# Kernel optimization log

Hardware: AMD Instinct MI355X
Metric: run time of the kernel (lower is better)

Reference implementation:

```python
import jax, jax.numpy as jnp
import numpy as np

N_NODES = 100000
N_EDGES = 1600000
HID = 32


def gcn_conv(x, W, b, src, dst, num_nodes):
    # PyG GCNConv: h = X W; out = D^{-1/2}(A+I)D^{-1/2} h + b
    # (self loops already appended to src/dst by caller)
    h = x @ W
    deg = jax.ops.segment_sum(jnp.ones_like(dst, dtype=h.dtype), dst,
                              num_segments=num_nodes)
    dinv = jnp.where(deg > 0, jax.lax.rsqrt(deg), 0.0)
    norm = dinv[src] * dinv[dst]                      # [E+N]
    msg = h[src] * norm[:, None]                      # gather + scale
    out = jax.ops.segment_sum(msg, dst, num_segments=num_nodes)  # scatter-add
    return out + b


def setup_inputs() -> dict:
    key = jax.random.key(0)
    ks = jax.random.split(key, 12)
    x = jax.random.normal(ks[0], (N_NODES, 2), dtype=jnp.float32)
    edge_index = jax.random.randint(ks[1], (2, N_EDGES), 0, N_NODES,
                                    dtype=jnp.int32)
    s = 0.2  # small init scale
    return {
        "x": x,
        "edge_index": edge_index,
        "fc1_W": jax.random.normal(ks[2], (2, HID), jnp.float32) * s,
        "fc1_b": jnp.zeros((HID,), jnp.float32),
        "c1_W": jax.random.normal(ks[3], (HID, HID), jnp.float32) * s,
        "c1_b": jnp.zeros((HID,), jnp.float32),
        "c2_W": jax.random.normal(ks[4], (HID, HID), jnp.float32) * s,
        "c2_b": jnp.zeros((HID,), jnp.float32),
        "c3_W": jax.random.normal(ks[5], (HID, HID), jnp.float32) * s,
        "c3_b": jnp.zeros((HID,), jnp.float32),
        "fc2_W": jax.random.normal(ks[6], (HID, HID), jnp.float32) * s,
        "fc2_b": jnp.zeros((HID,), jnp.float32),
        "fc3_W": jax.random.normal(ks[7], (HID, 1), jnp.float32) * s,
        "fc3_b": jnp.zeros((1,), jnp.float32),
    }


def reference(x, edge_index, fc1_W, fc1_b, c1_W, c1_b, c2_W, c2_b,
              c3_W, c3_b, fc2_W, fc2_b, fc3_W, fc3_b):
    num_nodes = x.shape[0]
    loop = jnp.arange(num_nodes, dtype=edge_index.dtype)
    src = jnp.concatenate([edge_index[0], loop])  # add self loops
    dst = jnp.concatenate([edge_index[1], loop])
    h = jax.nn.relu(x @ fc1_W + fc1_b)
    h = jax.nn.relu(gcn_conv(h, c1_W, c1_b, src, dst, num_nodes))
    h = jax.nn.relu(gcn_conv(h, c2_W, c2_b, src, dst, num_nodes))
    h = jax.nn.relu(gcn_conv(h, c3_W, c3_b, src, dst, num_nodes))
    h = jax.nn.relu(h @ fc2_W + fc2_b)
    return h @ fc3_W + fc3_b
```

## Files before the change

kernel.cpp:

```cpp
#include <hip/hip_runtime.h>
#include <hip/hip_fp16.h>

#define NN 100000
#define NE 1600000
#define HID 32
#define NBK 391
#define CAP 4608
#define CHUNK 8192

__device__ __forceinline__ float4 load_h4(const __half* p) {
    uint2 u = *(const uint2*)p;
    __half2 h0 = *(__half2*)&u.x;
    __half2 h1 = *(__half2*)&u.y;
    float2 a = __half22float2(h0);
    float2 b = __half22float2(h1);
    return make_float4(a.x, a.y, b.x, b.y);
}

__global__ __launch_bounds__(256) void partA_kernel(
        const int* __restrict__ src, const int* __restrict__ dst,
        int* __restrict__ bktcur, int* __restrict__ bedges) {
    __shared__ int cache[CHUNK];
    __shared__ int hist[NBK];
    __shared__ int lofs[NBK];
    int t = threadIdx.x;
    int base = blockIdx.x * CHUNK;
    for (int i = t; i < NBK; i += 256) hist[i] = 0;
    __syncthreads();
    for (int i = t; i < CHUNK; i += 256) {
        int e = base + i;
        if (e < NE) {
            int d = dst[e];
            cache[i] = d;
            atomicAdd(&hist[d >> 8], 1);
        }
    }
    __syncthreads();
    for (int i = t; i < NBK; i += 256)
        lofs[i] = hist[i] ? atomicAdd(&bktcur[i], hist[i]) : 0;
    __syncthreads();
    for (int i = t; i < CHUNK; i += 256) {
        int e = base + i;
        if (e < NE) {
            int d = cache[i];
            int s = src[e];
            int b = d >> 8;
            int rel = atomicAdd(&lofs[b], 1);
            if (rel < CAP) bedges[b * CAP + rel] = (s << 8) | (d & 255);
        }
    }
}

__global__ __launch_bounds__(256) void bucket_csr_kernel(
        const int* __restrict__ bedges, const int* __restrict__ bktcur,
        const float* __restrict__ x, float* __restrict__ dinv,
        int* __restrict__ srcidx, int* __restrict__ rbeg, int* __restrict__ rend,
        float4* __restrict__ xpack) {
    __shared__ int ldeg[256];
    __shared__ int lcur[256];
    __shared__ int wsum[256];
    int b = blockIdx.x, t = threadIdx.x;
    int ebeg = b * CAP;
    int cnt = min(bktcur[b], CAP);
    int n0 = b << 8;
    ldeg[t] = 0;
    __syncthreads();
    for (int e = t; e < cnt; e += 256)
        atomicAdd(&ldeg[bedges[ebeg + e] & 255], 1);
    __syncthreads();
    int a = ldeg[t];
    wsum[t] = a;
    __syncthreads();
    for (int off = 1; off < 256; off <<= 1) {
        int xv = (t >= off) ? wsum[t - off] : 0;
        __syncthreads();
        wsum[t] += xv;
        __syncthreads();
    }
    int excl = wsum[t] - a;
    lcur[t] = excl;
    int n = n0 + t;
    if (n < NN) {
        float dv = rsqrtf((float)(a + 1));
        rbeg[n] = ebeg + excl;
        rend[n] = ebeg + excl + a;
        dinv[n] = dv;
        float2 xv2 = *(const float2*)&x[2 * n];
        xpack[n] = make_float4(xv2.x, xv2.y, dv, 0.f);
    }
    __syncthreads();
    for (int e = t; e < cnt; e += 256) {
        int w = bedges[ebeg + e];
        int pos = atomicAdd(&lcur[w & 255], 1);
        srcidx[ebeg + pos] = (unsigned)w >> 8;
    }
}

__global__ __launch_bounds__(256) void conv1_kernel(
        const float4* __restrict__ xpack, const int* __restrict__ rbeg,
        const int* __restrict__ rend, const int* __restrict__ srcidx,
        const float* __restrict__ dinv, const float* __restrict__ W1,
        const float* __restrict__ b1, const float* __restrict__ W,
        const float* __restrict__ bias, __half* __restrict__ hs_out) {
    __shared__ float wl[HID * HID];
    __shared__ float agg[8][HID];
    int tid = threadIdx.x;
    int base8 = blockIdx.x * 8;
#pragma unroll
    for (int i = 0; i < 4; ++i) wl[tid + 256 * i] = W[tid + 256 * i];
    int wave = tid >> 6, lane = tid & 63;
    int g = lane >> 3;
    int l = lane & 7;
    float4 w0q = *(const float4*)&W1[l << 2];
    float4 w1q = *(const float4*)&W1[HID + (l << 2)];
    float4 bq  = *(const float4*)&b1[l << 2];
#pragma unroll
    for (int rep = 0; rep < 2; ++rep) {
        int ln = wave * 2 + rep;
        int n = base8 + ln;
        int beg = rbeg[n], end = rend[n];
        float4 acc0 = make_float4(0.f, 0.f, 0.f, 0.f);
        float4 acc1 = make_float4(0.f, 0.f, 0.f, 0.f);
        int e = beg + g;
        for (; e + 8 < end; e += 16) {
            float4 p0 = xpack[srcidx[e]];
            float4 p1 = xpack[srcidx[e + 8]];
            acc0.x += fmaxf(p0.x * w0q.x + p0.y * w1q.x + bq.x, 0.f) * p0.z;
            acc0.y += fmaxf(p0.x * w0q.y + p0.y * w1q.y + bq.y, 0.f) * p0.z;
            acc0.z += fmaxf(p0.x * w0q.z + p0.y * w1q.z + bq.z, 0.f) * p0.z;
            acc0.w += fmaxf(p0.x * w0q.w + p0.y * w1q.w + bq.w, 0.f) * p0.z;
            acc1.x += fmaxf(p1.x * w0q.x + p1.y * w1q.x + bq.x, 0.f) * p1.z;
            acc1.y += fmaxf(p1.x * w0q.y + p1.y * w1q.y + bq.y, 0.f) * p1.z;
            acc1.z += fmaxf(p1.x * w0q.z + p1.y * w1q.z + bq.z, 0.f) * p1.z;
            acc1.w += fmaxf(p1.x * w0q.w + p1.y * w1q.w + bq.w, 0.f) * p1.z;
        }
        if (e < end) {
            float4 p0 = xpack[srcidx[e]];
            acc0.x += fmaxf(p0.x * w0q.x + p0.y * w1q.x + bq.x, 0.f) * p0.z;
            acc0.y += fmaxf(p0.x * w0q.y + p0.y * w1q.y + bq.y, 0.f) * p0.z;
            acc0.z += fmaxf(p0.x * w0q.z + p0.y * w1q.z + bq.z, 0.f) * p0.z;
            acc0.w += fmaxf(p0.x * w0q.w + p0.y * w1q.w + bq.w, 0.f) * p0.z;
        }
        acc0.x += acc1.x; acc0.y += acc1.y; acc0.z += acc1.z; acc0.w += acc1.w;
#pragma unroll
        for (int m = 8; m < 64; m <<= 1) {
            acc0.x += __shfl_xor(acc0.x, m);
            acc0.y += __shfl_xor(acc0.y, m);
            acc0.z += __shfl_xor(acc0.z, m);
            acc0.w += __shfl_xor(acc0.w, m);
        }
        if (g == 0) {
            float4 ps = xpack[n];
            float dv = ps.z;
            float4 r;
            r.x = (acc0.x + fmaxf(ps.x * w0q.x + ps.y * w1q.x + bq.x, 0.f) * dv) * dv;
            r.y = (acc0.y + fmaxf(ps.x * w0q.y + ps.y * w1q.y + bq.y, 0.f) * dv) * dv;
            r.z = (acc0.z + fmaxf(ps.x * w0q.z + ps.y * w1q.z + bq.z, 0.f) * dv) * dv;
            r.w = (acc0.w + fmaxf(ps.x * w0q.w + ps.y * w1q.w + bq.w, 0.f) * dv) * dv;
            *(float4*)&agg[ln][l << 2] = r;
        }
    }
    __syncthreads();
    int ln = tid >> 5, j = tid & 31;
    int n = base8 + ln;
    float v = 0.f;
#pragma unroll
    for (int k = 0; k < HID; ++k) v += agg[ln][k] * wl[k * HID + j];
    v = fmaxf(v + bias[j], 0.f) * dinv[n];
    hs_out[(n << 5) + j] = __float2half(v);
}

template <bool OUTSCALE, bool FUSE23>
__global__ __launch_bounds__(256) void conv_fused_kernel(
        const __half* __restrict__ hs_in, const int* __restrict__ rbeg,
        const int* __restrict__ rend, const int* __restrict__ srcidx,
        const float* __restrict__ dinv, const float* __restrict__ W,
        const float* __restrict__ bias, const float* __restrict__ W2,
        const float* __restrict__ b2, const float* __restrict__ W3,
        const float* __restrict__ b3, void* __restrict__ hs_out_v) {
    __shared__ float wl[HID * HID];
    __shared__ float wl2[FUSE23 ? HID * HID : 1];
    __shared__ float agg[8][HID];
    int tid = threadIdx.x;
    int base8 = blockIdx.x * 8;
#pragma unroll
    for (int i = 0; i < 4; ++i) wl[tid + 256 * i] = W[tid + 256 * i];
    if (FUSE23) {
#pragma unroll
        for (int i = 0; i < 4; ++i) wl2[tid + 256 * i] = W2[tid + 256 * i];
    }
    int wave = tid >> 6, lane = tid & 63;
    int g = lane >> 3;
    int l = lane & 7;
#pragma unroll
    for (int rep = 0; rep < 2; ++rep) {
        int ln = wave * 2 + rep;
        int n = base8 + ln;
        int beg = rbeg[n], end = rend[n];
        float4 acc0 = make_float4(0.f, 0.f, 0.f, 0.f);
        float4 acc1 = make_float4(0.f, 0.f, 0.f, 0.f);
        int e = beg + g;
        for (; e + 8 < end; e += 16) {
            int s0 = srcidx[e];
            int s1 = srcidx[e + 8];
            float4 v0 = load_h4(&hs_in[(s0 << 5) + (l << 2)]);
            float4 v1 = load_h4(&hs_in[(s1 << 5) + (l << 2)]);
            acc0.x += v0.x; acc0.y += v0.y; acc0.z += v0.z; acc0.w += v0.w;
            acc1.x += v1.x; acc1.y += v1.y; acc1.z += v1.z; acc1.w += v1.w;
        }
        if (e < end) {
            int s0 = srcidx[e];
            float4 v0 = load_h4(&hs_in[(s0 << 5) + (l << 2)]);
            acc0.x += v0.x; acc0.y += v0.y; acc0.z += v0.z; acc0.w += v0.w;
        }
        acc0.x += acc1.x; acc0.y += acc1.y; acc0.z += acc1.z; acc0.w += acc1.w;
#pragma unroll
        for (int m = 8; m < 64; m <<= 1) {
            acc0.x += __shfl_xor(acc0.x, m);
            acc0.y += __shfl_xor(acc0.y, m);
            acc0.z += __shfl_xor(acc0.z, m);
            acc0.w += __shfl_xor(acc0.w, m);
        }
        if (g == 0) {
            float4 self = load_h4(&hs_in[(n << 5) + (l << 2)]);
            float dv = dinv[n];
            float4 r;
            r.x = (acc0.x + self.x) * dv;
            r.y = (acc0.y + self.y) * dv;
            r.z = (acc0.z + self.z) * dv;
            r.w = (acc0.w + self.w) * dv;
            *(float4*)&agg[ln][l << 2] = r;
        }
    }
    __syncthreads();
    int ln = tid >> 5, j = tid & 31;
    int n = base8 + ln;
    float v = 0.f;
#pragma unroll
    for (int k = 0; k < HID; ++k) v += agg[ln][k] * wl[k * HID + j];
    v = fmaxf(v + bias[j], 0.f);
    if (OUTSCALE) v *= dinv[n];
    if (!FUSE23) {
        ((__half*)hs_out_v)[(n << 5) + j] = __float2half(v);
    } else {
        __syncthreads();
        agg[ln][j] = v;
        __syncthreads();
        float v2 = 0.f;
#pragma unroll
        for (int k = 0; k < HID; ++k) v2 += agg[ln][k] * wl2[k * HID + j];
        v2 = fmaxf(v2 + b2[j], 0.f);
        float p = v2 * W3[j];
#pragma unroll
        for (int m = 16; m; m >>= 1) p += __shfl_xor(p, m);
        if (j == 0) ((float*)hs_out_v)[n] = p + b3[0];
    }
}

extern "C" void kernel_launch(void* const* d_in, const int* in_sizes, int n_in,
                              void* d_out, int out_size, void* d_ws, size_t ws_size,
                              hipStream_t stream) {
    const float* x     = (const float*)d_in[0];
    const int*   ei    = (const int*)d_in[1];
    const float* fc1_W = (const float*)d_in[2];
    const float* fc1_b = (const float*)d_in[3];
    const float* c1_W  = (const float*)d_in[4];
    const float* c1_b  = (const float*)d_in[5];
    const float* c2_W  = (const float*)d_in[6];
    const float* c2_b  = (const float*)d_in[7];
    const float* c3_W  = (const float*)d_in[8];
    const float* c3_b  = (const float*)d_in[9];
    const float* fc2_W = (const float*)d_in[10];
    const float* fc2_b = (const float*)d_in[11];
    const float* fc3_W = (const float*)d_in[12];
    const float* fc3_b = (const float*)d_in[13];

    const int* src = ei;
    const int* dst = ei + NE;

    float*  ws     = (float*)d_ws;
    float*  dinv   = ws;
    __half* hA     = (__half*)(ws + NN);
    __half* hB     = (__half*)(ws + NN + NN * HID);
    float4* xpack  = (float4*)(ws + NN + 2 * NN * HID);
    int*    srcidx = (int*)(xpack + NN);
    int*    rbeg   = srcidx + NBK * CAP;
    int*    rend   = rbeg + NN;
    int*    bktcur = rend + NN;
    int*    bedges = (int*)hB;

    float* out = (float*)d_out;

    const int B = 256;
    const int gNH = (NN * HID) / B;
    const int gPart = (NE + CHUNK - 1) / CHUNK;

    hipMemsetAsync(bktcur, 0, NBK * sizeof(int), stream);
    partA_kernel<<<gPart, B, 0, stream>>>(src, dst, bktcur, bedges);
    bucket_csr_kernel<<<NBK, B, 0, stream>>>(bedges, bktcur, x, dinv, srcidx, rbeg, rend, xpack);

    conv1_kernel<<<gNH, B, 0, stream>>>(xpack, rbeg, rend, srcidx, dinv,
                                        fc1_W, fc1_b, c1_W, c1_b, hA);
    conv_fused_kernel<true, false><<<gNH, B, 0, stream>>>(
        hA, rbeg, rend, srcidx, dinv, c2_W, c2_b, nullptr, nullptr, nullptr, nullptr, hB);
    conv_fused_kernel<false, true><<<gNH, B, 0, stream>>>(
        hB, rbeg, rend, srcidx, dinv, c3_W, c3_b, fc2_W, fc2_b, fc3_W, fc3_b, out);
}
```

Baseline: 181.6 us.

## Split fc2/fc3 into separate kernel, shrink partition chunk, macro-ize fc1 row math

Moves the fc2/fc3 head out of the last conv kernel into a standalone fc23 kernel, so conv3 writes its fp16 hidden state to a buffer and a new kernel reads it back. This removes the second weight tile and extra barriers from the conv kernel, which may lower its shared-memory use and raise occupancy, at the cost of an extra launch and a round trip of the hidden state through memory. It also reduces the edge-partition chunk from 8192 to 2048, giving more, smaller partA blocks. The fc1 arithmetic in conv1 is folded into a macro, and the self term is now added into the accumulator before scaling.

```diff
diff --git a/kernel.cpp b/kernel.cpp
--- a/kernel.cpp
+++ b/kernel.cpp
@@ -6,7 +6,7 @@
 #define HID 32
 #define NBK 391
 #define CAP 4608
-#define CHUNK 8192
+#define CHUNK 2048
 
 __device__ __forceinline__ float4 load_h4(const __half* p) {
     uint2 u = *(const uint2*)p;
@@ -114,6 +114,13 @@
     float4 w0q = *(const float4*)&W1[l << 2];
     float4 w1q = *(const float4*)&W1[HID + (l << 2)];
     float4 bq  = *(const float4*)&b1[l << 2];
+#define FC1ROW(dstacc, P)                                                      \
+    {                                                                          \
+        dstacc.x += fmaxf(P.x * w0q.x + P.y * w1q.x + bq.x, 0.f) * P.z;        \
+        dstacc.y += fmaxf(P.x * w0q.y + P.y * w1q.y + bq.y, 0.f) * P.z;        \
+        dstacc.z += fmaxf(P.x * w0q.z + P.y * w1q.z + bq.z, 0.f) * P.z;        \
+        dstacc.w += fmaxf(P.x * w0q.w + P.y * w1q.w + bq.w, 0.f) * P.z;        \
+    }
 #pragma unroll
     for (int rep = 0; rep < 2; ++rep) {
         int ln = wave * 2 + rep;
@@ -125,21 +132,12 @@
         for (; e + 8 < end; e += 16) {
             float4 p0 = xpack[srcidx[e]];
             float4 p1 = xpack[srcidx[e + 8]];
-            acc0.x += fmaxf(p0.x * w0q.x + p0.y * w1q.x + bq.x, 0.f) * p0.z;
-            acc0.y += fmaxf(p0.x * w0q.y + p0.y * w1q.y + bq.y, 0.f) * p0.z;
-            acc0.z += fmaxf(p0.x * w0q.z + p0.y * w1q.z + bq.z, 0.f) * p0.z;
-            acc0.w += fmaxf(p0.x * w0q.w + p0.y * w1q.w + bq.w, 0.f) * p0.z;
-            acc1.x += fmaxf(p1.x * w0q.x + p1.y * w1q.x + bq.x, 0.f) * p1.z;
-            acc1.y += fmaxf(p1.x * w0q.y + p1.y * w1q.y + bq.y, 0.f) * p1.z;
-            acc1.z += fmaxf(p1.x * w0q.z + p1.y * w1q.z + bq.z, 0.f) * p1.z;
-            acc1.w += fmaxf(p1.x * w0q.w + p1.y * w1q.w + bq.w, 0.f) * p1.z;
+            FC1ROW(acc0, p0);
+            FC1ROW(acc1, p1);
         }
         if (e < end) {
             float4 p0 = xpack[srcidx[e]];
-            acc0.x += fmaxf(p0.x * w0q.x + p0.y * w1q.x + bq.x, 0.f) * p0.z;
-            acc0.y += fmaxf(p0.x * w0q.y + p0.y * w1q.y + bq.y, 0.f) * p0.z;
-            acc0.z += fmaxf(p0.x * w0q.z + p0.y * w1q.z + bq.z, 0.f) * p0.z;
-            acc0.w += fmaxf(p0.x * w0q.w + p0.y * w1q.w + bq.w, 0.f) * p0.z;
+            FC1ROW(acc0, p0);
         }
         acc0.x += acc1.x; acc0.y += acc1.y; acc0.z += acc1.z; acc0.w += acc1.w;
 #pragma unroll
@@ -152,14 +150,12 @@
         if (g == 0) {
             float4 ps = xpack[n];
             float dv = ps.z;
-            float4 r;
-            r.x = (acc0.x + fmaxf(ps.x * w0q.x + ps.y * w1q.x + bq.x, 0.f) * dv) * dv;
-            r.y = (acc0.y + fmaxf(ps.x * w0q.y + ps.y * w1q.y + bq.y, 0.f) * dv) * dv;
-            r.z = (acc0.z + fmaxf(ps.x * w0q.z + ps.y * w1q.z + bq.z, 0.f) * dv) * dv;
-            r.w = (acc0.w + fmaxf(ps.x * w0q.w + ps.y * w1q.w + bq.w, 0.f) * dv) * dv;
-            *(float4*)&agg[ln][l << 2] = r;
-        }
-    }
+            FC1ROW(acc0, ps);
+            acc0.x *= dv; acc0.y *= dv; acc0.z *= dv; acc0.w *= dv;
+            *(float4*)&agg[ln][l << 2] = acc0;
+        }
+    }
+#undef FC1ROW
     __syncthreads();
     int ln = tid >> 5, j = tid & 31;
     int n = base8 + ln;
@@ -170,25 +166,18 @@
     hs_out[(n << 5) + j] = __float2half(v);
 }
 
-template <bool OUTSCALE, bool FUSE23>
+template <bool OUTSCALE>
 __global__ __launch_bounds__(256) void conv_fused_kernel(
         const __half* __restrict__ hs_in, const int* __restrict__ rbeg,
         const int* __restrict__ rend, const int* __restrict__ srcidx,
         const float* __restrict__ dinv, const float* __restrict__ W,
-        const float* __restrict__ bias, const float* __restrict__ W2,
-        const float* __restrict__ b2, const float* __restrict__ W3,
-        const float* __restrict__ b3, void* __restrict__ hs_out_v) {
+        const float* __restrict__ bias, __half* __restrict__ hs_out) {
     __shared__ float wl[HID * HID];
-    __shared__ float wl2[FUSE23 ? HID * HID : 1];
     __shared__ float agg[8][HID];
     int tid = threadIdx.x;
     int base8 = blockIdx.x * 8;
 #pragma unroll
     for (int i = 0; i < 4; ++i) wl[tid + 256 * i] = W[tid + 256 * i];
-    if (FUSE23) {
-#pragma unroll
-        for (int i = 0; i < 4; ++i) wl2[tid + 256 * i] = W2[tid + 256 * i];
-    }
     int wave = tid >> 6, lane = tid & 63;
     int g = lane >> 3;
     int l = lane & 7;
@@ -240,21 +229,30 @@
     for (int k = 0; k < HID; ++k) v += agg[ln][k] * wl[k * HID + j];
     v = fmaxf(v + bias[j], 0.f);
     if (OUTSCALE) v *= dinv[n];
-    if (!FUSE23) {
-        ((__half*)hs_out_v)[(n << 5) + j] = __float2half(v);
-    } else {
-        __syncthreads();
-        agg[ln][j] = v;
-        __syncthreads();
-        float v2 = 0.f;
-#pragma unroll
-        for (int k = 0; k < HID; ++k) v2 += agg[ln][k] * wl2[k * HID + j];
-        v2 = fmaxf(v2 + b2[j], 0.f);
-        float p = v2 * W3[j];
-#pragma unroll
-        for (int m = 16; m; m >>= 1) p += __shfl_xor(p, m);
-        if (j == 0) ((float*)hs_out_v)[n] = p + b3[0];
-    }
+    hs_out[(n << 5) + j] = __float2half(v);
+}
+
+__global__ __launch_bounds__(256) void fc23_kernel(
+        const __half* __restrict__ h, const float* __restrict__ W2,
+        const float* __restrict__ b2, const float* __restrict__ W3,
+        const float* __restrict__ b3, float* __restrict__ out) {
+    __shared__ float wl[HID * HID];
+    __shared__ float hsl[256];
+    int tid = threadIdx.x;
+    int base = blockIdx.x * 256;
+#pragma unroll
+    for (int i = 0; i < 4; ++i) wl[tid + 256 * i] = W2[tid + 256 * i];
+    hsl[tid] = __half2float(h[base + tid]);
+    __syncthreads();
+    int ln = tid >> 5, j = tid & 31;
+    float v = 0.f;
+#pragma unroll
+    for (int k = 0; k < HID; ++k) v += hsl[ln * HID + k] * wl[k * HID + j];
+    v = fmaxf(v + b2[j], 0.f);
+    float p = v * W3[j];
+#pragma unroll
+    for (int m = 16; m; m >>= 1) p += __shfl_xor(p, m);
+    if (j == 0) out[(base >> 5) + ln] = p + b3[0];
 }
 
 extern "C" void kernel_launch(void* const* d_in, const int* in_sizes, int n_in,
@@ -301,8 +299,9 @@
 
     conv1_kernel<<<gNH, B, 0, stream>>>(xpack, rbeg, rend, srcidx, dinv,
                                         fc1_W, fc1_b, c1_W, c1_b, hA);
-    conv_fused_kernel<true, false><<<gNH, B, 0, stream>>>(
-        hA, rbeg, rend, srcidx, dinv, c2_W, c2_b, nullptr, nullptr, nullptr, nullptr, hB);
-    conv_fused_kernel<false, true><<<gNH, B, 0, stream>>>(
-        hB, rbeg, rend, srcidx, dinv, c3_W, c3_b, fc2_W, fc2_b, fc3_W, fc3_b, out);
-}
+    conv_fused_kernel<true><<<gNH, B, 0, stream>>>(
+        hA, rbeg, rend, srcidx, dinv, c2_W, c2_b, hB);
+    conv_fused_kernel<false><<<gNH, B, 0, stream>>>(
+        hB, rbeg, rend, srcidx, dinv, c3_W, c3_b, hA);
+    fc23_kernel<<<gNH, B, 0, stream>>>(hA, fc2_W, fc2_b, fc3_W, fc3_b, out);
+}
```

Result: slower. 188.1 us (+3.6%).
